# Kernel optimization log

Measured on AMD Instinct MI355X. Metric: run time of the kernel, lower is better.

The kernel has to match this reference:

```python
import jax, jax.numpy as jnp
import numpy as np


def setup_inputs() -> dict:
    key = jax.random.key(0)
    k1, k2, k3, k4 = jax.random.split(key, 4)
    N, D, C = 131072, 128, 1024
    inputs = jax.random.normal(k1, (N, D), dtype=jnp.float32)
    centers = jax.random.normal(k2, (C, D), dtype=jnp.float32)
    gamma = jax.random.uniform(k3, (1,), dtype=jnp.float32)
    normalization = jax.random.normal(k4, (C, C), dtype=jnp.float32)
    return {"inputs": inputs, "centers": centers, "gamma": gamma,
            "normalization": normalization}


def _gaussian_kernel(inputs, centers, gamma):
    # Flatten trailing dims: [N, D]
    x = inputs.reshape(inputs.shape[0], -1)
    x2 = jnp.sum(x * x, axis=-1, keepdims=True)            # [N, 1]
    c2 = jnp.sum(centers * centers, axis=-1)               # [C]
    cross = x @ centers.T                                  # [N, C]
    sqd = jnp.maximum(x2 + c2[None, :] - 2.0 * cross, 0.0)  # [N, C]
    return jnp.exp(-gamma * sqd)


def reference(inputs, centers, gamma, normalization):
    densities = _gaussian_kernel(inputs, centers, gamma[0])  # [N, C]
    return densities @ normalization                          # [N, C]
```

## Files before the change

kernel.cpp:

```cpp
#include <hip/hip_runtime.h>
#include <hip/hip_fp8.h>
#include <stdint.h>

typedef float    f32x4  __attribute__((ext_vector_type(4)));
typedef float    f32x16 __attribute__((ext_vector_type(16)));
typedef int      i32x4  __attribute__((ext_vector_type(4)));
typedef int      i32x8  __attribute__((ext_vector_type(8)));
typedef __bf16   bf16x8 __attribute__((ext_vector_type(8)));
typedef uint16_t u16x8  __attribute__((ext_vector_type(8)));
typedef uint16_t u16x4  __attribute__((ext_vector_type(4)));
typedef uint8_t  u8x4   __attribute__((ext_vector_type(4)));
typedef uint32_t u32x4  __attribute__((ext_vector_type(4)));

static __device__ __forceinline__ f32x4 mfma_bf16(bf16x8 a, bf16x8 b, f32x4 c) {
  return __builtin_amdgcn_mfma_f32_16x16x32_bf16(a, b, c, 0, 0, 0);
}
static __device__ __forceinline__ uint16_t f2bf(float f) {
  uint32_t u = __builtin_bit_cast(uint32_t, f);
  u += 0x7fffu + ((u >> 16) & 1u);
  return (uint16_t)(u >> 16);
}
static __device__ __forceinline__ uint8_t f2fp8(float f) {
  __hip_fp8_e4m3 v(f);
  return v.__x;
}
static __device__ __forceinline__ void gload16(const void* src, void* lds) {
  __builtin_amdgcn_global_load_lds(
      (const __attribute__((address_space(1))) void*)src,
      (__attribute__((address_space(3))) void*)lds, 16, 0, 0);
}

constexpr int Nrows = 131072;
constexpr int Dk    = 128;
constexpr int Cc    = 1024;
constexpr int CH     = 16384;
constexpr int NCHUNK = Nrows / CH;
constexpr int BMf   = 64;
constexpr int BNf   = 256;
constexpr int KBf   = 128;
constexpr int XBYTES = BMf * Dk * 2;
constexpr int PBYTES = BMf * KBf * 2;
constexpr int LDS_MAIN = XBYTES + PBYTES + BMf * 4;
constexpr int LDS_FB   = LDS_MAIN + Cc * 4;
constexpr int KEXP2_LDS = 32768 * 3 + 128 * 144 + 512;

__global__ void prep_cen(const float* __restrict__ cen,
                         uint16_t* __restrict__ cenb,
                         float* __restrict__ c2) {
  const int t = threadIdx.x;
  const int row = blockIdx.x * 16 + (t >> 4);
  const int q = t & 15;
  const float* src = cen + (size_t)row * Dk + q * 8;
  f32x4 v0 = *(const f32x4*)src;
  f32x4 v1 = *(const f32x4*)(src + 4);
  u16x8 h;
  float ss = 0.f;
#pragma unroll
  for (int i = 0; i < 4; ++i) {
    h[i]     = f2bf(v0[i]); ss += v0[i] * v0[i];
    h[i + 4] = f2bf(v1[i]); ss += v1[i] * v1[i];
  }
  *(u16x8*)(cenb + (size_t)row * Dk + q * 8) = h;
  ss += __shfl_xor(ss, 1);
  ss += __shfl_xor(ss, 2);
  ss += __shfl_xor(ss, 4);
  ss += __shfl_xor(ss, 8);
  if (q == 0) c2[row] = ss;
}

__global__ void prep_nT8(const float* __restrict__ nrm, uint8_t* __restrict__ nT8) {
  __shared__ float tile[64][65];
  const int jb = blockIdx.x & 15;
  const int cb = blockIdx.x >> 4;
  const int t  = threadIdx.x;
  const int r  = t >> 4;
  const int q  = t & 15;
#pragma unroll
  for (int i = 0; i < 4; ++i) {
    int row = r + i * 16;
    f32x4 v = *(const f32x4*)(nrm + (size_t)(cb * 64 + row) * Cc + jb * 64 + q * 4);
#pragma unroll
    for (int s = 0; s < 4; ++s) tile[row][q * 4 + s] = v[s];
  }
  __syncthreads();
#pragma unroll
  for (int i = 0; i < 4; ++i) {
    int j = r + i * 16;
    u8x4 hs;
#pragma unroll
    for (int s = 0; s < 4; ++s) hs[s] = f2fp8(tile[q * 4 + s][j]);
    int sw  = (j >> 1) & 3;
    int col = cb * 64 + (((q >> 2) ^ sw) * 16) + (q & 3) * 4;
    *(u8x4*)(nT8 + (size_t)(jb * 64 + j) * Cc + col) = hs;
  }
}

__global__ void prep_nT(const float* __restrict__ nrm, uint16_t* __restrict__ nT) {
  __shared__ float tile[64][65];
  const int jb = blockIdx.x & 15;
  const int cb = blockIdx.x >> 4;
  const int t  = threadIdx.x;
  const int r  = t >> 4;
  const int q  = t & 15;
#pragma unroll
  for (int i = 0; i < 4; ++i) {
    int row = r + i * 16;
    f32x4 v = *(const f32x4*)(nrm + (size_t)(cb * 64 + row) * Cc + jb * 64 + q * 4);
#pragma unroll
    for (int s = 0; s < 4; ++s) tile[row][q * 4 + s] = v[s];
  }
  __syncthreads();
#pragma unroll
  for (int i = 0; i < 4; ++i) {
    int j = r + i * 16;
    u16x4 hs;
#pragma unroll
    for (int s = 0; s < 4; ++s) hs[s] = f2bf(tile[q * 4 + s][j]);
    *(u16x4*)(nT + (size_t)(jb * 64 + j) * Cc + cb * 64 + q * 4) = hs;
  }
}

__global__ __launch_bounds__(512, 2) void kexp2(
    const float* __restrict__ x, const float* __restrict__ gam,
    const uint16_t* __restrict__ cenb, const float* __restrict__ c2g,
    uint8_t* __restrict__ P, int row0) {
  extern __shared__ char smem[];
  char*    xB   = smem;
  char*    cB0  = smem + 32768;
  char*    cB1  = smem + 65536;
  uint8_t* pbuf = (uint8_t*)(smem + 98304);
  float*   x2s  = (float*)(smem + 98304 + 128 * 144);

  const int tid  = threadIdx.x;
  const int lane = tid & 63;
  const int wid  = tid >> 6;
  const int wr   = wid >> 2;
  const int wn   = wid & 3;
  const int l15  = lane & 15;
  const int l4   = lane >> 4;
  const int mb   = blockIdx.x;

  auto stage_c = [&](char* db, int ct) {
#pragma unroll
    for (int i = 0; i < 4; ++i) {
      int ch = tid + i * 512;
      int r  = ch >> 4;
      int c  = ch & 15;
      gload16(cenb + (size_t)(ct * 128 + r) * Dk + ((c ^ (r & 7)) * 8),
              db + ch * 16);
    }
  };
  stage_c(cB0, 0);

  const float* xblk = x + (size_t)(row0 + mb * 128) * Dk;
#pragma unroll
  for (int it = 0; it < 4; ++it) {
    int ch = tid + it * 512;
    int r  = ch >> 4;
    int cc = ch & 15;
    const float* src = xblk + r * Dk + cc * 8;
    f32x4 v0 = __builtin_nontemporal_load((const f32x4*)src);
    f32x4 v1 = __builtin_nontemporal_load((const f32x4*)(src + 4));
    u16x8 hh;
    float ss = 0.f;
#pragma unroll
    for (int i = 0; i < 4; ++i) {
      hh[i]     = f2bf(v0[i]); ss += v0[i] * v0[i];
      hh[i + 4] = f2bf(v1[i]); ss += v1[i] * v1[i];
    }
    *(u16x8*)(xB + r * 256 + ((cc ^ (r & 7)) * 16)) = hh;
    ss += __shfl_xor(ss, 1);
    ss += __shfl_xor(ss, 2);
    ss += __shfl_xor(ss, 4);
    ss += __shfl_xor(ss, 8);
    if ((tid & 15) == 0) x2s[r] = ss;
  }

  const float ngam = -gam[0];

  for (int ct = 0; ct < 8; ++ct) {
    char* cC = (ct & 1) ? cB1 : cB0;
    char* cN = (ct & 1) ? cB0 : cB1;
    if (ct < 7) stage_c(cN, ct + 1);
    if (ct == 0 || ct == 7) asm volatile("s_waitcnt vmcnt(4)" ::: "memory");
    else                    asm volatile("s_waitcnt vmcnt(8)" ::: "memory");
    __builtin_amdgcn_s_barrier();

    f32x4 cr[4][2];
#pragma unroll
    for (int m = 0; m < 4; ++m)
#pragma unroll
      for (int n = 0; n < 2; ++n) cr[m][n] = f32x4{0.f, 0.f, 0.f, 0.f};

#pragma unroll
    for (int kk = 0; kk < 4; ++kk) {
      bf16x8 aF[4], bF[2];
#pragma unroll
      for (int m = 0; m < 4; ++m) {
        int row = wr * 64 + m * 16 + l15;
        aF[m] = *(const bf16x8*)(xB + row * 256 +
                                 (((kk * 4 + l4) ^ (row & 7)) * 16));
      }
#pragma unroll
      for (int n = 0; n < 2; ++n) {
        int col = wn * 32 + n * 16 + l15;
        bF[n] = *(const bf16x8*)(cC + col * 256 +
                                 (((kk * 4 + l4) ^ (col & 7)) * 16));
      }
#pragma unroll
      for (int m = 0; m < 4; ++m)
#pragma unroll
        for (int n = 0; n < 2; ++n) cr[m][n] = mfma_bf16(aF[m], bF[n], cr[m][n]);
    }

    float c2v[2];
#pragma unroll
    for (int n = 0; n < 2; ++n) c2v[n] = c2g[ct * 128 + wn * 32 + n * 16 + l15];
#pragma unroll
    for (int m = 0; m < 4; ++m) {
#pragma unroll
      for (int n = 0; n < 2; ++n) {
#pragma unroll
        for (int rr = 0; rr < 4; ++rr) {
          int row = wr * 64 + m * 16 + l4 * 4 + rr;
          float s = fmaxf(fmaf(-2.f, cr[m][n][rr], x2s[row] + c2v[n]), 0.f);
          pbuf[row * 144 + wn * 32 + n * 16 + l15] = f2fp8(__expf(ngam * s));
        }
      }
    }
    __builtin_amdgcn_s_barrier();
#pragma unroll
    for (int it = 0; it < 2; ++it) {
      int ch = tid + it * 512;
      int r  = ch >> 3;
      int c  = ch & 7;
      int sw = (r >> 1) & 3;
      int dc = (c & 4) | ((c & 3) ^ sw);
      *(u32x4*)(P + (size_t)(mb * 128 + r) * Cc + ct * 128 + dc * 16) =
          *(const u32x4*)(pbuf + r * 144 + c * 16);
    }
  }
}

__global__ __launch_bounds__(512, 2) void g2f8(
    const uint8_t* __restrict__ P, const uint8_t* __restrict__ nT8,
    float* __restrict__ out, int row0, int mblocks) {
  extern __shared__ char smem[];
  char* a0 = smem;
  char* b0 = smem + 16384;
  char* a1 = smem + 32768;
  char* b1 = smem + 49152;

  const int tid  = threadIdx.x;
  const int lane = tid & 63;
  const int wid  = tid >> 6;
  const int wm   = wid >> 2;
  const int wn   = wid & 3;
  const int l31  = lane & 31;
  const int lh   = lane >> 5;

  const int nwg  = mblocks * 4;
  const int cpx  = nwg >> 3;
  const int wgid = (blockIdx.x & 7) * cpx + (blockIdx.x >> 3);
  const int nb   = wgid & 3;
  const int mb   = wgid >> 2;

  const uint8_t* Abase = P + (size_t)mb * 256 * Cc;
  const uint8_t* Bbase = nT8 + (size_t)nb * 256 * Cc;

  auto stage = [&](const uint8_t* gb, char* db, int k0) {
#pragma unroll
    for (int i = 0; i < 2; ++i) {
      int ch = tid + i * 512;
      int r  = ch >> 2;
      int c  = ch & 3;
      gload16(gb + (size_t)r * Cc + k0 + c * 16, db + ch * 16);
    }
  };

  int offA[4][2], offB[2][2];
#pragma unroll
  for (int m = 0; m < 4; ++m) {
    int row = wm * 128 + m * 32 + l31;
    int s = (row >> 1) & 3;
    offA[m][0] = row * 64 + ((2 * lh) ^ s) * 16;
    offA[m][1] = row * 64 + ((2 * lh + 1) ^ s) * 16;
  }
#pragma unroll
  for (int n = 0; n < 2; ++n) {
    int row = wn * 64 + n * 32 + l31;
    int s = (row >> 1) & 3;
    offB[n][0] = row * 64 + ((2 * lh) ^ s) * 16;
    offB[n][1] = row * 64 + ((2 * lh + 1) ^ s) * 16;
  }
  auto ldfrag = [&](const char* base, const int (&off)[2]) -> i32x8 {
    i32x4 lo = *(const i32x4*)(base + off[0]);
    i32x4 hi = *(const i32x4*)(base + off[1]);
    return __builtin_shufflevector(lo, hi, 0, 1, 2, 3, 4, 5, 6, 7);
  };

  f32x16 acc[4][2];
#pragma unroll
  for (int m = 0; m < 4; ++m)
#pragma unroll
    for (int n = 0; n < 2; ++n)
#pragma unroll
      for (int r = 0; r < 16; ++r) acc[m][n][r] = 0.f;

  stage(Bbase, b0, 0);
  stage(Abase, a0, 0);
  stage(Bbase, b1, 64);

  for (int kt = 0; kt < 16; ++kt) {
    const int q = kt & 1;
    char* aC = q ? a1 : a0;
    char* bC = q ? b1 : b0;
    char* aN = q ? a0 : a1;

    if (kt == 15) asm volatile("s_waitcnt vmcnt(0)" ::: "memory");
    else          asm volatile("s_waitcnt vmcnt(2)" ::: "memory");
    __builtin_amdgcn_s_barrier();

    if (kt + 1 < 16) stage(Abase, aN, (kt + 1) * 64);

    i32x8 bF[2];
#pragma unroll
    for (int n = 0; n < 2; ++n) bF[n] = ldfrag(bC, offB[n]);

    {
      i32x8 aF = ldfrag(aC, offA[0]);
      __builtin_amdgcn_s_setprio(1);
      acc[0][0] = __builtin_amdgcn_mfma_scale_f32_32x32x64_f8f6f4(
          aF, bF[0], acc[0][0], 0, 0, 0, 127, 0, 127);
      acc[0][1] = __builtin_amdgcn_mfma_scale_f32_32x32x64_f8f6f4(
          aF, bF[1], acc[0][1], 0, 0, 0, 127, 0, 127);
      __builtin_amdgcn_s_setprio(0);
    }
    __builtin_amdgcn_s_barrier();
    if (kt + 2 < 16) stage(Bbase, bC, (kt + 2) * 64);

    __builtin_amdgcn_s_setprio(1);
#pragma unroll
    for (int m = 1; m < 4; ++m) {
      i32x8 aF = ldfrag(aC, offA[m]);
      acc[m][0] = __builtin_amdgcn_mfma_scale_f32_32x32x64_f8f6f4(
          aF, bF[0], acc[m][0], 0, 0, 0, 127, 0, 127);
      acc[m][1] = __builtin_amdgcn_mfma_scale_f32_32x32x64_f8f6f4(
          aF, bF[1], acc[m][1], 0, 0, 0, 127, 0, 127);
    }
    __builtin_amdgcn_s_setprio(0);
  }

  float* obuf = (float*)smem;
#pragma unroll
  for (int h = 0; h < 4; ++h) {
    __syncthreads();
    if (wm == (h >> 1)) {
      const int mbase = (h & 1) * 2;
#pragma unroll
      for (int ml = 0; ml < 2; ++ml) {
#pragma unroll
        for (int n = 0; n < 2; ++n) {
#pragma unroll
          for (int r = 0; r < 16; ++r) {
            int rin = (r & 3) + 8 * (r >> 2) + 4 * lh;
            obuf[(ml * 32 + rin) * 256 + wn * 64 + n * 32 + l31] =
                acc[mbase + ml][n][r];
          }
        }
      }
    }
    __syncthreads();
#pragma unroll
    for (int i = 0; i < 8; ++i) {
      int ch = tid + i * 512;
      int rL = ch >> 6;
      int c4 = ch & 63;
      *(f32x4*)(out + (size_t)(row0 + mb * 256 + h * 64 + rL) * Cc +
                nb * 256 + c4 * 4) = *(const f32x4*)(obuf + rL * 256 + c4 * 4);
    }
  }
}

template <int USE_NT>
__global__ __launch_bounds__(512, 4) void nyst_main(
    const float* __restrict__ x, const float* __restrict__ cen,
    const float* __restrict__ gam, const float* __restrict__ nrm,
    const uint16_t* __restrict__ cenb, const float* __restrict__ c2g,
    const uint16_t* __restrict__ nT, float* __restrict__ out) {
  extern __shared__ char smem[];
  char*  xB  = smem;
  char*  pB  = smem + XBYTES;
  float* x2s = (float*)(smem + XBYTES + PBYTES);
  float* c2s = (float*)(smem + LDS_MAIN);

  const int tid  = threadIdx.x;
  const int lane = tid & 63;
  const int wid  = tid >> 6;
  const int wr   = wid >> 2;
  const int wc   = wid & 3;
  const int xcd  = blockIdx.x & 7;
  const int bi   = blockIdx.x >> 3;
  const int colb = xcd >> 1;
  const int rowb = (bi << 1) | (xcd & 1);
  const int l15  = lane & 15;
  const int l4   = lane >> 4;

  const float* xblk = x + (size_t)rowb * BMf * Dk;

#pragma unroll
  for (int it = 0; it < 2; ++it) {
    int ch = tid + it * 512;
    int r  = ch >> 4;
    int cc = ch & 15;
    const float* src = xblk + r * Dk + cc * 8;
    f32x4 v0 = __builtin_nontemporal_load((const f32x4*)src);
    f32x4 v1 = __builtin_nontemporal_load((const f32x4*)(src + 4));
    u16x8 hh;
    float ss = 0.f;
#pragma unroll
    for (int i = 0; i < 4; ++i) {
      hh[i]     = f2bf(v0[i]); ss += v0[i] * v0[i];
      hh[i + 4] = f2bf(v1[i]); ss += v1[i] * v1[i];
    }
    int off = (r * 256 + cc * 16) ^ ((r & 7) << 4);
    *(u16x8*)(xB + off) = hh;
    ss += __shfl_xor(ss, 1);
    ss += __shfl_xor(ss, 2);
    ss += __shfl_xor(ss, 4);
    ss += __shfl_xor(ss, 8);
    if ((tid & 15) == 0) x2s[r] = ss;
  }
  if (!USE_NT) {
#pragma unroll
    for (int rr = 0; rr < 2; ++rr) {
      int r = tid + rr * 512;
      const float* src = cen + (size_t)r * Dk;
      float ss = 0.f;
      for (int k = 0; k < Dk / 4; ++k) {
        f32x4 v = *(const f32x4*)(src + 4 * k);
        ss += v[0] * v[0] + v[1] * v[1] + v[2] * v[2] + v[3] * v[3];
      }
      c2s[r] = ss;
    }
  }
  __syncthreads();

  const float ngam = -gam[0];
  f32x4 zero4 = {0.f, 0.f, 0.f, 0.f};
  f32x4 acc[2][4];
#pragma unroll
  for (int m = 0; m < 2; ++m)
#pragma unroll
    for (int n = 0; n < 4; ++n) acc[m][n] = zero4;

  for (int c0 = 0; c0 < Cc; c0 += KBf) {
    f32x4 cr[2][2];
#pragma unroll
    for (int g = 0; g < 2; ++g)
#pragma unroll
      for (int m = 0; m < 2; ++m) cr[g][m] = zero4;

#pragma unroll
    for (int kk = 0; kk < 4; ++kk) {
      bf16x8 b0, b1;
      if (USE_NT) {
        int c0col = c0 + 16 * wc + l15;
        b0 = *(const bf16x8*)(cenb + (size_t)c0col * Dk + kk * 32 + l4 * 8);
        b1 = *(const bf16x8*)(cenb + (size_t)(c0col + 64) * Dk + kk * 32 + l4 * 8);
      } else {
#pragma unroll
        for (int g = 0; g < 2; ++g) {
          int ccol = c0 + g * 64 + 16 * wc + l15;
          const float* cb_ = cen + (size_t)ccol * Dk + kk * 32 + l4 * 8;
          f32x4 v0 = *(const f32x4*)cb_;
          f32x4 v1 = *(const f32x4*)(cb_ + 4);
          u16x8 tt;
#pragma unroll
          for (int i = 0; i < 4; ++i) { tt[i] = f2bf(v0[i]); tt[i + 4] = f2bf(v1[i]); }
          if (g == 0) b0 = __builtin_bit_cast(bf16x8, tt);
          else        b1 = __builtin_bit_cast(bf16x8, tt);
        }
      }
#pragma unroll
      for (int m = 0; m < 2; ++m) {
        int row = 32 * wr + 16 * m + l15;
        int off = (row * 256 + kk * 64 + l4 * 16) ^ ((row & 7) << 4);
        bf16x8 a = *(const bf16x8*)(xB + off);
        cr[0][m] = mfma_bf16(a, b0, cr[0][m]);
        cr[1][m] = mfma_bf16(a, b1, cr[1][m]);
      }
    }

    __syncthreads();
#pragma unroll
    for (int g = 0; g < 2; ++g) {
      int ccol = c0 + g * 64 + 16 * wc + l15;
      float c2v = USE_NT ? c2g[ccol] : c2s[ccol];
#pragma unroll
      for (int m = 0; m < 2; ++m) {
#pragma unroll
        for (int r = 0; r < 4; ++r) {
          int row = 32 * wr + 16 * m + l4 * 4 + r;
          float s = fmaxf(fmaf(-2.f, cr[g][m][r], x2s[row] + c2v), 0.f);
          float p = __expf(ngam * s);
          int off = (row * 256 + (g * 64 + 16 * wc + l15) * 2) ^ ((row & 7) << 4);
          *(uint16_t*)(pB + off) = f2bf(p);
        }
      }
    }
    __syncthreads();

#pragma unroll
    for (int kk = 0; kk < 4; ++kk) {
      bf16x8 pa[2];
#pragma unroll
      for (int m = 0; m < 2; ++m) {
        int row = 32 * wr + 16 * m + l15;
        int off = (row * 256 + kk * 64 + l4 * 16) ^ ((row & 7) << 4);
        pa[m] = *(const bf16x8*)(pB + off);
      }
      int krow = c0 + kk * 32 + l4 * 8;
#pragma unroll
      for (int n = 0; n < 4; ++n) {
        int j = colb * BNf + wc * 64 + 16 * n + l15;
        bf16x8 bm;
        if (USE_NT) {
          bm = *(const bf16x8*)(nT + (size_t)j * Cc + krow);
        } else {
          u16x8 tt;
#pragma unroll
          for (int i = 0; i < 8; ++i) tt[i] = f2bf(nrm[(size_t)(krow + i) * Cc + j]);
          bm = __builtin_bit_cast(bf16x8, tt);
        }
        acc[0][n] = mfma_bf16(pa[0], bm, acc[0][n]);
        acc[1][n] = mfma_bf16(pa[1], bm, acc[1][n]);
      }
    }
  }

  float* outBuf = (float*)smem;
  const int orow0 = rowb * BMf;
#pragma unroll
  for (int h = 0; h < 2; ++h) {
    __syncthreads();
    if (wr == h) {
#pragma unroll
      for (int m = 0; m < 2; ++m) {
#pragma unroll
        for (int n = 0; n < 4; ++n) {
#pragma unroll
          for (int r = 0; r < 4; ++r) {
            int rL = 16 * m + l4 * 4 + r;
            outBuf[rL * 256 + wc * 64 + 16 * n + l15] = acc[m][n][r];
          }
        }
      }
    }
    __syncthreads();
#pragma unroll
    for (int i = 0; i < 4; ++i) {
      int ch = tid + 512 * i;
      int rL = ch >> 6;
      int c4 = ch & 63;
      f32x4 v = *(const f32x4*)(outBuf + rL * 256 + c4 * 4);
      *(f32x4*)(out + (size_t)(orow0 + 32 * h + rL) * Cc + colb * BNf + c4 * 4) = v;
    }
  }
}

extern "C" void kernel_launch(void* const* d_in, const int* in_sizes, int n_in,
                              void* d_out, int out_size, void* d_ws, size_t ws_size,
                              hipStream_t stream) {
  const float* x   = (const float*)d_in[0];
  const float* cen = (const float*)d_in[1];
  const float* gam = (const float*)d_in[2];
  const float* nrm = (const float*)d_in[3];
  float* out = (float*)d_out;

  const size_t cenbB = (size_t)Cc * Dk * 2;
  const size_t c2B   = (size_t)Cc * 4;
  const size_t nT8B  = (size_t)Cc * Cc;
  const size_t nTB   = (size_t)Cc * Cc * 2;
  const size_t pFull = (size_t)Nrows * Cc;
  const size_t pChB  = (size_t)CH * Cc;

  if (ws_size >= cenbB + c2B + nT8B + pFull) {
    uint16_t* cenb = (uint16_t*)d_ws;
    float*    c2   = (float*)((char*)d_ws + cenbB);
    uint8_t*  nT8  = (uint8_t*)((char*)d_ws + cenbB + c2B);
    uint8_t*  Pws  = (uint8_t*)((char*)d_ws + cenbB + c2B + nT8B);
    prep_cen<<<64, 256, 0, stream>>>(cen, cenb, c2);
    prep_nT8<<<256, 256, 0, stream>>>(nrm, nT8);
    kexp2<<<Nrows / 128, 512, KEXP2_LDS, stream>>>(x, gam, cenb, c2, Pws, 0);
    g2f8<<<(Nrows / 256) * 4, 512, 65536, stream>>>(Pws, nT8, out, 0, Nrows / 256);
  } else if (ws_size >= cenbB + c2B + nT8B + pChB) {
    uint16_t* cenb = (uint16_t*)d_ws;
    float*    c2   = (float*)((char*)d_ws + cenbB);
    uint8_t*  nT8  = (uint8_t*)((char*)d_ws + cenbB + c2B);
    uint8_t*  Pws  = (uint8_t*)((char*)d_ws + cenbB + c2B + nT8B);
    prep_cen<<<64, 256, 0, stream>>>(cen, cenb, c2);
    prep_nT8<<<256, 256, 0, stream>>>(nrm, nT8);
    for (int c = 0; c < NCHUNK; ++c) {
      kexp2<<<CH / 128, 512, KEXP2_LDS, stream>>>(x, gam, cenb, c2, Pws, c * CH);
      g2f8<<<(CH / 256) * 4, 512, 65536, stream>>>(Pws, nT8, out, c * CH, CH / 256);
    }
  } else if (ws_size >= cenbB + c2B + nTB) {
    uint16_t* cenb = (uint16_t*)d_ws;
    float*    c2   = (float*)((char*)d_ws + cenbB);
    uint16_t* nT   = (uint16_t*)((char*)d_ws + cenbB + c2B);
    prep_cen<<<64, 256, 0, stream>>>(cen, cenb, c2);
    prep_nT<<<256, 256, 0, stream>>>(nrm, nT);
    nyst_main<1><<<(Nrows / BMf) * (Cc / BNf), 512, LDS_MAIN, stream>>>(
        x, cen, gam, nrm, cenb, c2, nT, out);
  } else {
    nyst_main<0><<<(Nrows / BMf) * (Cc / BNf), 512, LDS_FB, stream>>>(
        x, cen, gam, nrm, nullptr, nullptr, nullptr, out);
  }
}
```

Measured before the change: 320.1 us.

## Keep full A panel resident in LDS and loop over all output column blocks

The fp8 GEMM kernel now has each workgroup load a 128-row slice of P (all 1024 K) into LDS once. It then iterates over the four 256-column blocks of the normalization matrix, streaming only B tiles and writing each output block in turn. Before, the grid covered (m-block, n-block) pairs, so each P row was read from global memory four times; this change removes those repeated reads. The costs are 160KB of LDS per block, which cuts occupancy, a serial A load that no compute overlaps, and a 1024-byte LDS row stride that may cause bank conflicts on A fragment reads.

```diff
diff --git a/kernel.cpp b/kernel.cpp
--- a/kernel.cpp
+++ b/kernel.cpp
@@ -43,6 +43,7 @@
 constexpr int LDS_MAIN = XBYTES + PBYTES + BMf * 4;
 constexpr int LDS_FB   = LDS_MAIN + Cc * 4;
 constexpr int KEXP2_LDS = 32768 * 3 + 128 * 144 + 512;
+constexpr int G2F8_LDS  = 131072 + 2 * 16384;
 
 __global__ void prep_cen(const float* __restrict__ cen,
                          uint16_t* __restrict__ cenb,
@@ -244,12 +245,11 @@
 
 __global__ __launch_bounds__(512, 2) void g2f8(
     const uint8_t* __restrict__ P, const uint8_t* __restrict__ nT8,
-    float* __restrict__ out, int row0, int mblocks) {
+    float* __restrict__ out, int row0) {
   extern __shared__ char smem[];
-  char* a0 = smem;
-  char* b0 = smem + 16384;
-  char* a1 = smem + 32768;
-  char* b1 = smem + 49152;
+  char* aS = smem;
+  char* b0 = smem + 131072;
+  char* b1 = smem + 147456;
 
   const int tid  = threadIdx.x;
   const int lane = tid & 63;
@@ -258,33 +258,26 @@
   const int wn   = wid & 3;
   const int l31  = lane & 31;
   const int lh   = lane >> 5;
-
-  const int nwg  = mblocks * 4;
-  const int cpx  = nwg >> 3;
-  const int wgid = (blockIdx.x & 7) * cpx + (blockIdx.x >> 3);
-  const int nb   = wgid & 3;
-  const int mb   = wgid >> 2;
-
-  const uint8_t* Abase = P + (size_t)mb * 256 * Cc;
-  const uint8_t* Bbase = nT8 + (size_t)nb * 256 * Cc;
-
-  auto stage = [&](const uint8_t* gb, char* db, int k0) {
+  const int mb   = blockIdx.x;
+
+  const uint8_t* Abase = P + (size_t)mb * 128 * Cc;
+
+  auto stageB = [&](char* db, int nb, int k0) {
 #pragma unroll
     for (int i = 0; i < 2; ++i) {
       int ch = tid + i * 512;
-      int r  = ch >> 2;
-      int c  = ch & 3;
-      gload16(gb + (size_t)r * Cc + k0 + c * 16, db + ch * 16);
+      int r  = ch >> 2, c = ch & 3;
+      gload16(nT8 + (size_t)(nb * 256 + r) * Cc + k0 + c * 16, db + ch * 16);
     }
   };
 
-  int offA[4][2], offB[2][2];
-#pragma unroll
-  for (int m = 0; m < 4; ++m) {
-    int row = wm * 128 + m * 32 + l31;
+  int offA0[2][2], offB[2][2];
+#pragma unroll
+  for (int m = 0; m < 2; ++m) {
+    int row = wm * 64 + m * 32 + l31;
     int s = (row >> 1) & 3;
-    offA[m][0] = row * 64 + ((2 * lh) ^ s) * 16;
-    offA[m][1] = row * 64 + ((2 * lh + 1) ^ s) * 16;
+    offA0[m][0] = row * 1024 + ((2 * lh) ^ s) * 16;
+    offA0[m][1] = row * 1024 + ((2 * lh + 1) ^ s) * 16;
   }
 #pragma unroll
   for (int n = 0; n < 2; ++n) {
@@ -293,92 +286,91 @@
     offB[n][0] = row * 64 + ((2 * lh) ^ s) * 16;
     offB[n][1] = row * 64 + ((2 * lh + 1) ^ s) * 16;
   }
-  auto ldfrag = [&](const char* base, const int (&off)[2]) -> i32x8 {
-    i32x4 lo = *(const i32x4*)(base + off[0]);
-    i32x4 hi = *(const i32x4*)(base + off[1]);
-    return __builtin_shufflevector(lo, hi, 0, 1, 2, 3, 4, 5, 6, 7);
-  };
-
-  f32x16 acc[4][2];
-#pragma unroll
-  for (int m = 0; m < 4; ++m)
+
+  f32x16 acc[2][2];
+#pragma unroll
+  for (int m = 0; m < 2; ++m)
 #pragma unroll
     for (int n = 0; n < 2; ++n)
 #pragma unroll
       for (int r = 0; r < 16; ++r) acc[m][n][r] = 0.f;
 
-  stage(Bbase, b0, 0);
-  stage(Abase, a0, 0);
-  stage(Bbase, b1, 64);
-
-  for (int kt = 0; kt < 16; ++kt) {
-    const int q = kt & 1;
-    char* aC = q ? a1 : a0;
-    char* bC = q ? b1 : b0;
-    char* aN = q ? a0 : a1;
-
-    if (kt == 15) asm volatile("s_waitcnt vmcnt(0)" ::: "memory");
-    else          asm volatile("s_waitcnt vmcnt(2)" ::: "memory");
-    __builtin_amdgcn_s_barrier();
-
-    if (kt + 1 < 16) stage(Abase, aN, (kt + 1) * 64);
-
-    i32x8 bF[2];
-#pragma unroll
-    for (int n = 0; n < 2; ++n) bF[n] = ldfrag(bC, offB[n]);
-
-    {
-      i32x8 aF = ldfrag(aC, offA[0]);
+#pragma unroll
+  for (int i = 0; i < 16; ++i) {
+    int ch = tid + i * 512;
+    gload16(Abase + ch * 16, aS + ch * 16);
+  }
+  stageB(b0, 0, 0);
+  stageB(b1, 0, 64);
+  asm volatile("s_waitcnt vmcnt(0)" ::: "memory");
+  __builtin_amdgcn_s_barrier();
+
+  for (int nb = 0; nb < 4; ++nb) {
+    if (nb > 0) {
+      stageB(b0, nb, 0);
+      stageB(b1, nb, 64);
+    }
+    for (int kt = 0; kt < 16; ++kt) {
+      char* bC = (kt & 1) ? b1 : b0;
+      if (kt >= 14) asm volatile("s_waitcnt vmcnt(0)" ::: "memory");
+      else          asm volatile("s_waitcnt vmcnt(2)" ::: "memory");
+      __builtin_amdgcn_s_barrier();
+
+      i32x8 bF[2];
+#pragma unroll
+      for (int n = 0; n < 2; ++n) {
+        i32x4 lo = *(const i32x4*)(bC + offB[n][0]);
+        i32x4 hi = *(const i32x4*)(bC + offB[n][1]);
+        bF[n] = __builtin_shufflevector(lo, hi, 0, 1, 2, 3, 4, 5, 6, 7);
+      }
       __builtin_amdgcn_s_setprio(1);
-      acc[0][0] = __builtin_amdgcn_mfma_scale_f32_32x32x64_f8f6f4(
-          aF, bF[0], acc[0][0], 0, 0, 0, 127, 0, 127);
-      acc[0][1] = __builtin_amdgcn_mfma_scale_f32_32x32x64_f8f6f4(
-          aF, bF[1], acc[0][1], 0, 0, 0, 127, 0, 127);
+#pragma unroll
+      for (int m = 0; m < 2; ++m) {
+        i32x4 lo = *(const i32x4*)(aS + offA0[m][0] + kt * 64);
+        i32x4 hi = *(const i32x4*)(aS + offA0[m][1] + kt * 64);
+        i32x8 aF = __builtin_shufflevector(lo, hi, 0, 1, 2, 3, 4, 5, 6, 7);
+        acc[m][0] = __builtin_amdgcn_mfma_scale_f32_32x32x64_f8f6f4(
+            aF, bF[0], acc[m][0], 0, 0, 0, 127, 0, 127);
+        acc[m][1] = __builtin_amdgcn_mfma_scale_f32_32x32x64_f8f6f4(
+            aF, bF[1], acc[m][1], 0, 0, 0, 127, 0, 127);
+      }
       __builtin_amdgcn_s_setprio(0);
-    }
-    __builtin_amdgcn_s_barrier();
-    if (kt + 2 < 16) stage(Bbase, bC, (kt + 2) * 64);
-
-    __builtin_amdgcn_s_setprio(1);
-#pragma unroll
-    for (int m = 1; m < 4; ++m) {
-      i32x8 aF = ldfrag(aC, offA[m]);
-      acc[m][0] = __builtin_amdgcn_mfma_scale_f32_32x32x64_f8f6f4(
-          aF, bF[0], acc[m][0], 0, 0, 0, 127, 0, 127);
-      acc[m][1] = __builtin_amdgcn_mfma_scale_f32_32x32x64_f8f6f4(
-          aF, bF[1], acc[m][1], 0, 0, 0, 127, 0, 127);
-    }
-    __builtin_amdgcn_s_setprio(0);
-  }
-
-  float* obuf = (float*)smem;
-#pragma unroll
-  for (int h = 0; h < 4; ++h) {
-    __syncthreads();
-    if (wm == (h >> 1)) {
-      const int mbase = (h & 1) * 2;
-#pragma unroll
-      for (int ml = 0; ml < 2; ++ml) {
+      __builtin_amdgcn_s_barrier();
+      if (kt + 2 < 16) stageB(bC, nb, (kt + 2) * 64);
+    }
+
+    float* obuf = (float*)(smem + 131072);
+#pragma unroll
+    for (int h = 0; h < 4; ++h) {
+      __syncthreads();
+      if (wm == (h >> 1)) {
+        const int m = h & 1;
 #pragma unroll
         for (int n = 0; n < 2; ++n) {
 #pragma unroll
           for (int r = 0; r < 16; ++r) {
             int rin = (r & 3) + 8 * (r >> 2) + 4 * lh;
-            obuf[(ml * 32 + rin) * 256 + wn * 64 + n * 32 + l31] =
-                acc[mbase + ml][n][r];
+            obuf[rin * 256 + wn * 64 + n * 32 + l31] = acc[m][n][r];
           }
         }
       }
+      __syncthreads();
+#pragma unroll
+      for (int i = 0; i < 4; ++i) {
+        int ch = tid + i * 512;
+        int rL = ch >> 6;
+        int c4 = ch & 63;
+        *(f32x4*)(out + (size_t)(row0 + mb * 128 + h * 32 + rL) * Cc +
+                  nb * 256 + c4 * 4) = *(const f32x4*)(obuf + rL * 256 + c4 * 4);
+      }
     }
     __syncthreads();
 #pragma unroll
-    for (int i = 0; i < 8; ++i) {
-      int ch = tid + i * 512;
-      int rL = ch >> 6;
-      int c4 = ch & 63;
-      *(f32x4*)(out + (size_t)(row0 + mb * 256 + h * 64 + rL) * Cc +
-                nb * 256 + c4 * 4) = *(const f32x4*)(obuf + rL * 256 + c4 * 4);
-    }
+    for (int m = 0; m < 2; ++m)
+#pragma unroll
+      for (int n = 0; n < 2; ++n)
+#pragma unroll
+        for (int r = 0; r < 16; ++r) acc[m][n][r] = 0.f;
   }
 }
 
@@ -593,7 +585,7 @@
     prep_cen<<<64, 256, 0, stream>>>(cen, cenb, c2);
     prep_nT8<<<256, 256, 0, stream>>>(nrm, nT8);
     kexp2<<<Nrows / 128, 512, KEXP2_LDS, stream>>>(x, gam, cenb, c2, Pws, 0);
-    g2f8<<<(Nrows / 256) * 4, 512, 65536, stream>>>(Pws, nT8, out, 0, Nrows / 256);
+    g2f8<<<Nrows / 128, 512, G2F8_LDS, stream>>>(Pws, nT8, out, 0);
   } else if (ws_size >= cenbB + c2B + nT8B + pChB) {
     uint16_t* cenb = (uint16_t*)d_ws;
     float*    c2   = (float*)((char*)d_ws + cenbB);
@@ -603,7 +595,7 @@
     prep_nT8<<<256, 256, 0, stream>>>(nrm, nT8);
     for (int c = 0; c < NCHUNK; ++c) {
       kexp2<<<CH / 128, 512, KEXP2_LDS, stream>>>(x, gam, cenb, c2, Pws, c * CH);
-      g2f8<<<(CH / 256) * 4, 512, 65536, stream>>>(Pws, nT8, out, c * CH, CH / 256);
+      g2f8<<<CH / 128, 512, G2F8_LDS, stream>>>(Pws, nT8, out, c * CH);
     }
   } else if (ws_size >= cenbB + c2B + nTB) {
     uint16_t* cenb = (uint16_t*)d_ws;
```

Result: slower. 789.8 us (+146.7%).

## Double g2f8 K-tile to 128 with 8-way XOR swizzle layout

Applied to the files above, without the earlier changes.

Widens the FP8 GEMM k-step from 64 to 128 bytes per stage, halving the number of loop iterations and barriers. Each iteration issues twice as many MFMAs. The P and nT8 producers are changed to write a matching 8-chunk XOR swizzle, and the fragment offsets are updated to match. LDS per block grows to 128KB, which likely limits the kernel to one workgroup per CU instead of two.

```diff
diff --git a/kernel.cpp b/kernel.cpp
--- a/kernel.cpp
+++ b/kernel.cpp
@@ -43,6 +43,7 @@
 constexpr int LDS_MAIN = XBYTES + PBYTES + BMf * 4;
 constexpr int LDS_FB   = LDS_MAIN + Cc * 4;
 constexpr int KEXP2_LDS = 32768 * 3 + 128 * 144 + 512;
+constexpr int G2F8_LDS  = 131072;
 
 __global__ void prep_cen(const float* __restrict__ cen,
                          uint16_t* __restrict__ cenb,
@@ -89,8 +90,9 @@
     u8x4 hs;
 #pragma unroll
     for (int s = 0; s < 4; ++s) hs[s] = f2fp8(tile[q * 4 + s][j]);
-    int sw  = (j >> 1) & 3;
-    int col = cb * 64 + (((q >> 2) ^ sw) * 16) + (q & 3) * 4;
+    int c   = ((cb & 1) << 2) | (q >> 2);
+    int dc  = c ^ (j & 7);
+    int col = (cb >> 1) * 128 + dc * 16 + (q & 3) * 4;
     *(u8x4*)(nT8 + (size_t)(jb * 64 + j) * Cc + col) = hs;
   }
 }
@@ -234,8 +236,7 @@
       int ch = tid + it * 512;
       int r  = ch >> 3;
       int c  = ch & 7;
-      int sw = (r >> 1) & 3;
-      int dc = (c & 4) | ((c & 3) ^ sw);
+      int dc = c ^ (r & 7);
       *(u32x4*)(P + (size_t)(mb * 128 + r) * Cc + ct * 128 + dc * 16) =
           *(const u32x4*)(pbuf + r * 144 + c * 16);
     }
@@ -247,9 +248,9 @@
     float* __restrict__ out, int row0, int mblocks) {
   extern __shared__ char smem[];
   char* a0 = smem;
-  char* b0 = smem + 16384;
-  char* a1 = smem + 32768;
-  char* b1 = smem + 49152;
+  char* b0 = smem + 32768;
+  char* a1 = smem + 65536;
+  char* b1 = smem + 98304;
 
   const int tid  = threadIdx.x;
   const int lane = tid & 63;
@@ -270,28 +271,34 @@
 
   auto stage = [&](const uint8_t* gb, char* db, int k0) {
 #pragma unroll
-    for (int i = 0; i < 2; ++i) {
+    for (int i = 0; i < 4; ++i) {
       int ch = tid + i * 512;
-      int r  = ch >> 2;
-      int c  = ch & 3;
+      int r  = ch >> 3;
+      int c  = ch & 7;
       gload16(gb + (size_t)r * Cc + k0 + c * 16, db + ch * 16);
     }
   };
 
-  int offA[4][2], offB[2][2];
+  int offA[4][2][2], offB[2][2][2];
 #pragma unroll
   for (int m = 0; m < 4; ++m) {
     int row = wm * 128 + m * 32 + l31;
-    int s = (row >> 1) & 3;
-    offA[m][0] = row * 64 + ((2 * lh) ^ s) * 16;
-    offA[m][1] = row * 64 + ((2 * lh + 1) ^ s) * 16;
+    int s = row & 7;
+#pragma unroll
+    for (int g = 0; g < 2; ++g)
+#pragma unroll
+      for (int j = 0; j < 2; ++j)
+        offA[m][g][j] = row * 128 + (((g * 4 + 2 * lh + j) ^ s) * 16);
   }
 #pragma unroll
   for (int n = 0; n < 2; ++n) {
     int row = wn * 64 + n * 32 + l31;
-    int s = (row >> 1) & 3;
-    offB[n][0] = row * 64 + ((2 * lh) ^ s) * 16;
-    offB[n][1] = row * 64 + ((2 * lh + 1) ^ s) * 16;
+    int s = row & 7;
+#pragma unroll
+    for (int g = 0; g < 2; ++g)
+#pragma unroll
+      for (int j = 0; j < 2; ++j)
+        offB[n][g][j] = row * 128 + (((g * 4 + 2 * lh + j) ^ s) * 16);
   }
   auto ldfrag = [&](const char* base, const int (&off)[2]) -> i32x8 {
     i32x4 lo = *(const i32x4*)(base + off[0]);
@@ -309,45 +316,50 @@
 
   stage(Bbase, b0, 0);
   stage(Abase, a0, 0);
-  stage(Bbase, b1, 64);
-
-  for (int kt = 0; kt < 16; ++kt) {
+  stage(Bbase, b1, 128);
+
+  for (int kt = 0; kt < 8; ++kt) {
     const int q = kt & 1;
     char* aC = q ? a1 : a0;
     char* bC = q ? b1 : b0;
     char* aN = q ? a0 : a1;
 
-    if (kt == 15) asm volatile("s_waitcnt vmcnt(0)" ::: "memory");
-    else          asm volatile("s_waitcnt vmcnt(2)" ::: "memory");
+    if (kt == 7) asm volatile("s_waitcnt vmcnt(0)" ::: "memory");
+    else         asm volatile("s_waitcnt vmcnt(4)" ::: "memory");
     __builtin_amdgcn_s_barrier();
 
-    if (kt + 1 < 16) stage(Abase, aN, (kt + 1) * 64);
-
-    i32x8 bF[2];
-#pragma unroll
-    for (int n = 0; n < 2; ++n) bF[n] = ldfrag(bC, offB[n]);
-
-    {
-      i32x8 aF = ldfrag(aC, offA[0]);
-      __builtin_amdgcn_s_setprio(1);
+    if (kt + 1 < 8) stage(Abase, aN, (kt + 1) * 128);
+
+    i32x8 bF[2][2];
+#pragma unroll
+    for (int n = 0; n < 2; ++n)
+#pragma unroll
+      for (int g = 0; g < 2; ++g) bF[n][g] = ldfrag(bC, offB[n][g]);
+
+    __builtin_amdgcn_s_setprio(1);
+#pragma unroll
+    for (int g = 0; g < 2; ++g) {
+      i32x8 aF = ldfrag(aC, offA[0][g]);
       acc[0][0] = __builtin_amdgcn_mfma_scale_f32_32x32x64_f8f6f4(
-          aF, bF[0], acc[0][0], 0, 0, 0, 127, 0, 127);
+          aF, bF[0][g], acc[0][0], 0, 0, 0, 127, 0, 127);
       acc[0][1] = __builtin_amdgcn_mfma_scale_f32_32x32x64_f8f6f4(
-          aF, bF[1], acc[0][1], 0, 0, 0, 127, 0, 127);
-      __builtin_amdgcn_s_setprio(0);
-    }
+          aF, bF[1][g], acc[0][1], 0, 0, 0, 127, 0, 127);
+    }
+    __builtin_amdgcn_s_setprio(0);
     __builtin_amdgcn_s_barrier();
-    if (kt + 2 < 16) stage(Bbase, bC, (kt + 2) * 64);
+    if (kt + 2 < 8) stage(Bbase, bC, (kt + 2) * 128);
 
     __builtin_amdgcn_s_setprio(1);
 #pragma unroll
-    for (int m = 1; m < 4; ++m) {
-      i32x8 aF = ldfrag(aC, offA[m]);
-      acc[m][0] = __builtin_amdgcn_mfma_scale_f32_32x32x64_f8f6f4(
-          aF, bF[0], acc[m][0], 0, 0, 0, 127, 0, 127);
-      acc[m][1] = __builtin_amdgcn_mfma_scale_f32_32x32x64_f8f6f4(
-          aF, bF[1], acc[m][1], 0, 0, 0, 127, 0, 127);
-    }
+    for (int m = 1; m < 4; ++m)
+#pragma unroll
+      for (int g = 0; g < 2; ++g) {
+        i32x8 aF = ldfrag(aC, offA[m][g]);
+        acc[m][0] = __builtin_amdgcn_mfma_scale_f32_32x32x64_f8f6f4(
+            aF, bF[0][g], acc[m][0], 0, 0, 0, 127, 0, 127);
+        acc[m][1] = __builtin_amdgcn_mfma_scale_f32_32x32x64_f8f6f4(
+            aF, bF[1][g], acc[m][1], 0, 0, 0, 127, 0, 127);
+      }
     __builtin_amdgcn_s_setprio(0);
   }
 
@@ -593,7 +605,7 @@
     prep_cen<<<64, 256, 0, stream>>>(cen, cenb, c2);
     prep_nT8<<<256, 256, 0, stream>>>(nrm, nT8);
     kexp2<<<Nrows / 128, 512, KEXP2_LDS, stream>>>(x, gam, cenb, c2, Pws, 0);
-    g2f8<<<(Nrows / 256) * 4, 512, 65536, stream>>>(Pws, nT8, out, 0, Nrows / 256);
+    g2f8<<<(Nrows / 256) * 4, 512, G2F8_LDS, stream>>>(Pws, nT8, out, 0, Nrows / 256);
   } else if (ws_size >= cenbB + c2B + nT8B + pChB) {
     uint16_t* cenb = (uint16_t*)d_ws;
     float*    c2   = (float*)((char*)d_ws + cenbB);
@@ -603,7 +615,7 @@
     prep_nT8<<<256, 256, 0, stream>>>(nrm, nT8);
     for (int c = 0; c < NCHUNK; ++c) {
       kexp2<<<CH / 128, 512, KEXP2_LDS, stream>>>(x, gam, cenb, c2, Pws, c * CH);
-      g2f8<<<(CH / 256) * 4, 512, 65536, stream>>>(Pws, nT8, out, c * CH, CH / 256);
+      g2f8<<<(CH / 256) * 4, 512, G2F8_LDS, stream>>>(Pws, nT8, out, c * CH, CH / 256);
     }
   } else if (ws_size >= cenbB + c2B + nTB) {
     uint16_t* cenb = (uint16_t*)d_ws;
```

New measurement: 308.2 us (median of 3 runs). 3.7% less time.
